# Performance work log

Measured on AMD Instinct MI355X. Metric: run time of the kernel, lower is better.

Reference implementation:

```python
import jax, jax.numpy as jnp
import numpy as np

N_NODES = 50000
N_EDGES = 300000
N_GRAPHS = 256
F_IN = 78
H1 = 10
F_H1 = 78
F_OUT = 128
NEG_SLOPE = 0.2  # PyG GATConv default leaky_relu slope


def gat_conv(x, src, dst, W, a_src, a_dst, bias, heads, out_dim):
    """PyG GATConv (eval mode): linear -> per-edge attention -> segment softmax over
    destination nodes -> scatter-add aggregation -> concat heads + bias.
    src/dst already include self-loops."""
    N = x.shape[0]
    h = (x @ W).reshape(N, heads, out_dim)              # [N,H,F]
    al_s = (h * a_src[None]).sum(-1)                     # [N,H]
    al_d = (h * a_dst[None]).sum(-1)                     # [N,H]
    e = jax.nn.leaky_relu(al_s[src] + al_d[dst], NEG_SLOPE)  # [E,H]
    m = jax.ops.segment_max(e, dst, num_segments=N)      # stable softmax per dst node
    w = jnp.exp(e - m[dst])
    denom = jax.ops.segment_sum(w, dst, num_segments=N)
    alpha = w / denom[dst]                               # [E,H]
    out = jax.ops.segment_sum(h[src] * alpha[:, :, None], dst, num_segments=N)
    return out.reshape(N, heads * out_dim) + bias


def setup_inputs() -> dict:
    key = jax.random.key(0)
    ks = jax.random.split(key, 16)
    x = jax.random.normal(ks[0], (N_NODES, F_IN), dtype=jnp.float32)
    edge_index = jax.random.randint(ks[1], (2, N_EDGES), 0, N_NODES, dtype=jnp.int32)
    batch = jnp.sort(jax.random.randint(ks[2], (N_NODES,), 0, N_GRAPHS, dtype=jnp.int32))
    s = 0.1
    W1 = jax.random.normal(ks[3], (F_IN, H1 * F_H1), dtype=jnp.float32) * s
    a_src1 = jax.random.normal(ks[4], (H1, F_H1), dtype=jnp.float32) * s
    a_dst1 = jax.random.normal(ks[5], (H1, F_H1), dtype=jnp.float32) * s
    b1 = jnp.zeros((H1 * F_H1,), dtype=jnp.float32)
    W2 = jax.random.normal(ks[6], (H1 * F_H1, F_OUT), dtype=jnp.float32) * s
    a_src2 = jax.random.normal(ks[7], (1, F_OUT), dtype=jnp.float32) * s
    a_dst2 = jax.random.normal(ks[8], (1, F_OUT), dtype=jnp.float32) * s
    b2 = jnp.zeros((F_OUT,), dtype=jnp.float32)
    fc_w = jax.random.normal(ks[9], (F_OUT, F_OUT), dtype=jnp.float32) * s
    fc_b = jnp.zeros((F_OUT,), dtype=jnp.float32)
    return dict(x=x, edge_index=edge_index, batch=batch, W1=W1, a_src1=a_src1,
                a_dst1=a_dst1, b1=b1, W2=W2, a_src2=a_src2, a_dst2=a_dst2, b2=b2,
                fc_w=fc_w, fc_b=fc_b)


def reference(x, edge_index, batch, W1, a_src1, a_dst1, b1, W2, a_src2, a_dst2, b2, fc_w, fc_b):
    N = x.shape[0]
    loop = jnp.arange(N, dtype=edge_index.dtype)
    src = jnp.concatenate([edge_index[0], loop])  # add self-loops (PyG default)
    dst = jnp.concatenate([edge_index[1], loop])
    # dropout layers are identity in eval mode
    h = jax.nn.elu(gat_conv(x, src, dst, W1, a_src1, a_dst1, b1, H1, F_H1))
    h = gat_conv(h, src, dst, W2, a_src2, a_dst2, b2, 1, F_OUT)
    h = jax.nn.relu(h)
    g = jax.ops.segment_max(h, batch, num_segments=N_GRAPHS)  # global max pool [B,F]
    out = jax.nn.relu(g @ fc_w + fc_b)
    return out
```

## Files before the change

kernel.cpp:

```cpp
#include <hip/hip_runtime.h>
#include <hip/hip_bf16.h>

#define N_NODES 50000
#define N_EDGES 300000
#define E_TOT   350000
#define N_GRAPHS 256
#define F_IN 78
#define H1 10
#define D1 780
#define F_OUT 128
#define KP 800
#define K1P 96
#define O1P 808
#define NEG_SLOPE 0.2f
#define NB 196

typedef float v4f __attribute__((ext_vector_type(4)));
typedef short v8s __attribute__((ext_vector_type(8)));

__device__ __forceinline__ int src_of(int e, const int* __restrict__ ei) {
  return (e < N_EDGES) ? ei[e] : (e - N_EDGES);
}
__device__ __forceinline__ int dst_of(int e, const int* __restrict__ ei) {
  return (e < N_EDGES) ? ei[N_EDGES + e] : (e - N_EDGES);
}
__device__ __forceinline__ float bf2f(unsigned short u) {
  return __uint_as_float(((unsigned int)u) << 16);
}


__global__ void k_deg(const int* __restrict__ ei, int* __restrict__ deg) {
  int e = blockIdx.x * 256 + threadIdx.x;
  if (e >= E_TOT) return;
  atomicAdd(&deg[dst_of(e, ei)], 1);
}

__global__ void k_scan1(const int* __restrict__ deg, int* __restrict__ part) {
  __shared__ int s[256];
  int t = threadIdx.x;
  int i = blockIdx.x * 256 + t;
  s[t] = (i < N_NODES) ? deg[i] : 0;
  __syncthreads();
  for (int d = 128; d > 0; d >>= 1) {
    if (t < d) s[t] += s[t + d];
    __syncthreads();
  }
  if (t == 0) part[blockIdx.x] = s[0];
}

__global__ void k_scan2(const int* __restrict__ part, int* __restrict__ ppref) {
  if (threadIdx.x == 0) {
    int run = 0;
    for (int i = 0; i < NB; ++i) { ppref[i] = run; run += part[i]; }
  }
}

__global__ void k_scan3(const int* __restrict__ deg, const int* __restrict__ ppref,
                        int* __restrict__ offs, int* __restrict__ cursor) {
  __shared__ int s[256];
  int t = threadIdx.x;
  int i = blockIdx.x * 256 + t;
  int v = (i < N_NODES) ? deg[i] : 0;
  s[t] = v;
  __syncthreads();
  for (int d = 1; d < 256; d <<= 1) {
    int u = (t >= d) ? s[t - d] : 0;
    __syncthreads();
    s[t] += u;
    __syncthreads();
  }
  int excl = s[t] - v;
  if (i < N_NODES) {
    int off = ppref[blockIdx.x] + excl;
    offs[i] = off;
    cursor[i] = off;
  }
}

__global__ void k_scatter(const int* __restrict__ ei, int* __restrict__ cursor,
                          int* __restrict__ src_s, int* __restrict__ dst_s) {
  int e = blockIdx.x * 256 + threadIdx.x;
  if (e >= E_TOT) return;
  int s = src_of(e, ei);
  int d = dst_of(e, ei);
  int pos = atomicAdd(&cursor[d], 1);
  src_s[pos] = s;
  dst_s[pos] = d;
}


__global__ void k_xb(const float* __restrict__ x, __hip_bfloat16* __restrict__ xb) {
  int i = blockIdx.x * 256 + threadIdx.x;
  if (i >= N_NODES * F_IN) return;
  xb[i] = __float2bfloat16(x[i]);
}


__global__ void k_prep(const float* __restrict__ W1, const float* __restrict__ as1,
                       const float* __restrict__ ad1, float* __restrict__ was,
                       float* __restrict__ wad) {
  int i = blockIdx.x * 256 + threadIdx.x;
  if (i >= F_IN * H1) return;
  int k = i / H1, h = i - k * H1;
  const float* wrow = W1 + (size_t)k * D1 + h * 78;
  const float* ar = as1 + h * 78;
  const float* br = ad1 + h * 78;
  float s = 0.f, d = 0.f;
  for (int f = 0; f < 78; ++f) {
    float w = wrow[f];
    s = fmaf(w, ar[f], s);
    d = fmaf(w, br[f], d);
  }
  was[i] = s;
  wad[i] = d;
}


__global__ __launch_bounds__(320) void k_logits1(const float* __restrict__ x,
                                                 const float* __restrict__ was,
                                                 const float* __restrict__ wad,
                                                 float* __restrict__ als,
                                                 float* __restrict__ ald) {
  __shared__ float xs[32][81];
  __shared__ float wl[D1], wl2[D1];
  int tid = threadIdx.x;
  int n0 = blockIdx.x * 32;
  for (int i = tid; i < 32 * F_IN; i += 320) {
    int r = i / F_IN, k = i - r * F_IN;
    int n = n0 + r;
    xs[r][k] = (n < N_NODES) ? x[(size_t)n * F_IN + k] : 0.f;
  }
  for (int i = tid; i < D1; i += 320) { wl[i] = was[i]; wl2[i] = wad[i]; }
  __syncthreads();
  int r = tid / 10, h = tid - r * 10;
  int n = n0 + r;
  float s = 0.f, d = 0.f;
  for (int k = 0; k < F_IN; ++k) {
    float xv = xs[r][k];
    s = fmaf(xv, wl[k * 10 + h], s);
    d = fmaf(xv, wl2[k * 10 + h], d);
  }
  if (n < N_NODES) { als[n * 10 + h] = s; ald[n * 10 + h] = d; }
}


__global__ void k_w1e(const float* __restrict__ als1, const float* __restrict__ ald1,
                      const int* __restrict__ src_s, const int* __restrict__ dst_s,
                      float* __restrict__ w1) {
  int i = blockIdx.x * 256 + threadIdx.x;
  if (i >= E_TOT * H1) return;
  int pos = i / H1, h = i - pos * H1;
  float v = als1[src_s[pos] * H1 + h] + ald1[dst_s[pos] * H1 + h];
  v = (v > 0.f) ? v : NEG_SLOPE * v;
  w1[i] = __expf(v);
}


__global__ void k_w1t(const float* __restrict__ W1, __hip_bfloat16* __restrict__ T) {
  int i = blockIdx.x * 256 + threadIdx.x;
  if (i >= 800 * K1P) return;
  int r = i / K1P, k = i - r * K1P;
  float v = (r < D1 && k < F_IN) ? W1[(size_t)k * D1 + r] : 0.f;
  T[i] = __float2bfloat16(v);
}


__global__ void k_w2t(const float* __restrict__ W2, __hip_bfloat16* __restrict__ Bt) {
  int i = blockIdx.x * 256 + threadIdx.x;
  if (i >= F_OUT * KP) return;
  int c = i / KP, k = i - c * KP;
  float v = (k < D1) ? W2[(size_t)k * F_OUT + c] : 0.f;
  Bt[i] = __float2bfloat16(v);
}


__global__ __launch_bounds__(512, 4) void k_l12(const __hip_bfloat16* __restrict__ xb16,
                                                const float* __restrict__ w1,
                                                const int* __restrict__ src_s,
                                                const int* __restrict__ offs,
                                                const int* __restrict__ deg,
                                                const __hip_bfloat16* __restrict__ W1T,
                                                const float* __restrict__ b1,
                                                const __hip_bfloat16* __restrict__ W2T,
                                                const float* __restrict__ a_src2,
                                                const float* __restrict__ a_dst2,
                                                __hip_bfloat16* __restrict__ h2b,
                                                float* __restrict__ als2,
                                                float* __restrict__ ald2) {
  __shared__ __align__(16) unsigned char lds[34048];
  __hip_bfloat16* xbb = (__hip_bfloat16*)lds;
  __hip_bfloat16* out1t = (__hip_bfloat16*)lds;
  float* h2t = (float*)(lds + 25856);
#define XB(h, g, k) xbb[((h) * 16 + (g)) * 104 + (k)]

  int tid = threadIdx.x, wid = tid >> 6, lane = tid & 63;
  int n0 = blockIdx.x * 16;
  int col16 = lane & 15, kq = (lane >> 4) * 8;

  {
    unsigned int* p = (unsigned int*)lds;
    for (int i = tid; i < H1 * 16 * 52; i += 512) p[i] = 0u;
  }
  __syncthreads();

  #pragma unroll
  for (int rep = 0; rep < 2; ++rep) {
    int g = wid * 2 + rep;
    int n = n0 + g;
    int o = __builtin_amdgcn_readfirstlane(offs[n]);
    int d = __builtin_amdgcn_readfirstlane(deg[n]);
    float acc[H1], acc2[H1];
    #pragma unroll
    for (int h = 0; h < H1; ++h) { acc[h] = 0.f; acc2[h] = 0.f; }

    float onesel = (lane == 14) ? 1.0f : 0.f;
    const unsigned short* xu = (const unsigned short*)xb16;
    int j = 0;
    for (; j + 4 <= d; j += 4) {
      int e0 = o + j;
      int s0 = src_s[e0], s1 = src_s[e0 + 1], s2 = src_s[e0 + 2], s3 = src_s[e0 + 3];
      const unsigned short* x0 = xu + (size_t)s0 * F_IN;
      const unsigned short* x1 = xu + (size_t)s1 * F_IN;
      const unsigned short* x2 = xu + (size_t)s2 * F_IN;
      const unsigned short* x3 = xu + (size_t)s3 * F_IN;
      float xa0 = bf2f(x0[lane]), xa1 = bf2f(x1[lane]);
      float xa2 = bf2f(x2[lane]), xa3 = bf2f(x3[lane]);
      float xb0 = (lane < 14) ? bf2f(x0[64 + lane]) : onesel;
      float xb1 = (lane < 14) ? bf2f(x1[64 + lane]) : onesel;
      float xb2 = (lane < 14) ? bf2f(x2[64 + lane]) : onesel;
      float xb3 = (lane < 14) ? bf2f(x3[64 + lane]) : onesel;
      const float* wp = w1 + (size_t)e0 * H1;
      #pragma unroll
      for (int h = 0; h < H1; ++h) {
        float wa = wp[h], wb = wp[10 + h], wc = wp[20 + h], wd = wp[30 + h];
        acc[h] = fmaf(wa, xa0, acc[h]);
        acc[h] = fmaf(wb, xa1, acc[h]);
        acc[h] = fmaf(wc, xa2, acc[h]);
        acc[h] = fmaf(wd, xa3, acc[h]);
        acc2[h] = fmaf(wa, xb0, acc2[h]);
        acc2[h] = fmaf(wb, xb1, acc2[h]);
        acc2[h] = fmaf(wc, xb2, acc2[h]);
        acc2[h] = fmaf(wd, xb3, acc2[h]);
      }
    }
    for (; j < d; ++j) {
      int e0 = o + j;
      int s0 = src_s[e0];
      const unsigned short* x0 = xu + (size_t)s0 * F_IN;
      float xa0 = bf2f(x0[lane]);
      float xb0 = (lane < 14) ? bf2f(x0[64 + lane]) : onesel;
      const float* wp = w1 + (size_t)e0 * H1;
      #pragma unroll
      for (int h = 0; h < H1; ++h) {
        float wa = wp[h];
        acc[h] = fmaf(wa, xa0, acc[h]);
        acc2[h] = fmaf(wa, xb0, acc2[h]);
      }
    }
    #pragma unroll
    for (int h = 0; h < H1; ++h) {
      float inv = 1.f / __shfl(acc2[h], 14);
      XB(h, g, lane) = __float2bfloat16(acc[h] * inv);
      if (lane < 14) XB(h, g, 64 + lane) = __float2bfloat16(acc2[h] * inv);
    }
  }
  __syncthreads();

  const unsigned short* Bp1 = (const unsigned short*)W1T;
  v4f res[7];
  #pragma unroll
  for (int i = 0; i < 7; ++i) {
    int u = wid + i * 8;
    v4f acc = (v4f){0.f, 0.f, 0.f, 0.f};
    if (u < 50) {
      int h = u / 5, nt = u - (u / 5) * 5;
      #pragma unroll
      for (int kt = 0; kt < 3; ++kt) {
        v8s a = *reinterpret_cast<const v8s*>(&XB(h, col16, kt * 32 + kq));
        v8s b = *reinterpret_cast<const v8s*>(
            &Bp1[(size_t)(h * 78 + nt * 16 + col16) * K1P + kt * 32 + kq]);
        acc = __builtin_amdgcn_mfma_f32_16x16x32_bf16(a, b, acc, 0, 0, 0);
      }
    }
    res[i] = acc;
  }
  __syncthreads();

  if (tid < 224) {
    int node = tid / 14, cc = (tid - node * 14) * 2;
    *(unsigned int*)&out1t[node * O1P + 780 + cc] = 0u;
  }
  #pragma unroll
  for (int i = 0; i < 7; ++i) {
    int u = wid + i * 8;
    if (u < 50) {
      int h = u / 5, nt = u - (u / 5) * 5;
      v4f acc = res[i];
      int cl = nt * 16 + col16;
      if (cl < 78) {
        int c = h * 78 + cl;
        float bv = b1[c];
        #pragma unroll
        for (int r = 0; r < 4; ++r) {
          int node = (lane >> 4) * 4 + r;
          float v = acc[r] + bv;
          v = (v > 0.f) ? v : expm1f(v);
          out1t[node * O1P + c] = __float2bfloat16(v);
        }
      }
    }
  }
  __syncthreads();

  const unsigned short* Bp2 = (const unsigned short*)W2T;
  v4f acc3 = (v4f){0.f, 0.f, 0.f, 0.f};
  #pragma unroll 5
  for (int kt = 0; kt < 25; ++kt) {
    int k = kt * 32 + kq;
    v8s a = *reinterpret_cast<const v8s*>(&out1t[col16 * O1P + k]);
    v8s b = *reinterpret_cast<const v8s*>(&Bp2[(size_t)(wid * 16 + col16) * KP + k]);
    acc3 = __builtin_amdgcn_mfma_f32_16x16x32_bf16(a, b, acc3, 0, 0, 0);
  }
  {
    int col = wid * 16 + col16;
    #pragma unroll
    for (int r = 0; r < 4; ++r) {
      int node = (lane >> 4) * 4 + r;
      h2b[(size_t)(n0 + node) * F_OUT + col] = __float2bfloat16(acc3[r]);
      h2t[node * F_OUT + col] = acc3[r];
    }
  }
  __syncthreads();

  #pragma unroll
  for (int rep = 0; rep < 2; ++rep) {
    int nn = wid * 2 + rep;
    float v0 = h2t[nn * F_OUT + lane], v1 = h2t[nn * F_OUT + 64 + lane];
    float s = v0 * a_src2[lane] + v1 * a_src2[64 + lane];
    float dd = v0 * a_dst2[lane] + v1 * a_dst2[64 + lane];
    #pragma unroll
    for (int off = 32; off > 0; off >>= 1) {
      s += __shfl_down(s, off);
      dd += __shfl_down(dd, off);
    }
    if (lane == 0) { als2[n0 + nn] = s; ald2[n0 + nn] = dd; }
  }
#undef XB
}


__global__ void k_w2e(const float* __restrict__ als2, const float* __restrict__ ald2,
                      const int* __restrict__ src_s, const int* __restrict__ dst_s,
                      float* __restrict__ w2) {
  int pos = blockIdx.x * 256 + threadIdx.x;
  if (pos >= E_TOT) return;
  float v = als2[src_s[pos]] + ald2[dst_s[pos]];
  v = (v > 0.f) ? v : NEG_SLOPE * v;
  w2[pos] = __expf(v);
}


__global__ __launch_bounds__(512) void k_agg2f(const __hip_bfloat16* __restrict__ h2b,
                                               const float* __restrict__ w2,
                                               const int* __restrict__ src_s,
                                               const int* __restrict__ offs,
                                               const int* __restrict__ deg,
                                               const float* __restrict__ b2,
                                               const int* __restrict__ batch,
                                               unsigned int* __restrict__ g) {
  int tid = threadIdx.x;
  int n = blockIdx.x * 4 + (tid >> 7);
  int f = tid & 127;
  int o = __builtin_amdgcn_readfirstlane(offs[n]);
  int d = __builtin_amdgcn_readfirstlane(deg[n]);
  const unsigned short* hu = (const unsigned short*)h2b;
  float acc = 0.f, ssum = 0.f;
  int j = 0;
  for (; j + 4 <= d; j += 4) {
    float wq[4], hq[4];
    #pragma unroll
    for (int q = 0; q < 4; ++q) {
      int e = o + j + q;
      wq[q] = w2[e];
      hq[q] = bf2f(hu[(size_t)src_s[e] * F_OUT + f]);
    }
    #pragma unroll
    for (int q = 0; q < 4; ++q) {
      ssum += wq[q];
      acc = fmaf(wq[q], hq[q], acc);
    }
  }
  for (; j < d; ++j) {
    int e = o + j;
    float w = w2[e];
    ssum += w;
    acc = fmaf(w, bf2f(hu[(size_t)src_s[e] * F_OUT + f]), acc);
  }
  float v = fmaxf(acc / ssum + b2[f], 0.f);
  int gc = __builtin_amdgcn_readfirstlane(batch[n]);
  atomicMax(&g[gc * F_OUT + f], __float_as_uint(v));
}


__global__ __launch_bounds__(128) void k_fc(const float* __restrict__ g,
                                            const float* __restrict__ fc_w,
                                            const float* __restrict__ fc_b,
                                            float* __restrict__ out) {
  int b = blockIdx.x, c = threadIdx.x;
  const float* gr = g + (size_t)b * F_OUT;
  float acc = 0.f;
  for (int k = 0; k < F_OUT; ++k) acc = fmaf(gr[k], fc_w[k * F_OUT + c], acc);
  float v = acc + fc_b[c];
  out[(size_t)b * F_OUT + c] = fmaxf(v, 0.f);
}


extern "C" void kernel_launch(void* const* d_in, const int* in_sizes, int n_in,
                              void* d_out, int out_size, void* d_ws, size_t ws_size,
                              hipStream_t stream) {
  const float* x      = (const float*)d_in[0];
  const int*   ei     = (const int*)  d_in[1];
  const int*   batch  = (const int*)  d_in[2];
  const float* W1     = (const float*)d_in[3];
  const float* a_src1 = (const float*)d_in[4];
  const float* a_dst1 = (const float*)d_in[5];
  const float* b1     = (const float*)d_in[6];
  const float* W2     = (const float*)d_in[7];
  const float* a_src2 = (const float*)d_in[8];
  const float* a_dst2 = (const float*)d_in[9];
  const float* b2     = (const float*)d_in[10];
  const float* fc_w   = (const float*)d_in[11];
  const float* fc_b   = (const float*)d_in[12];
  float* out = (float*)d_out;

  float* ws = (float*)d_ws;
  __hip_bfloat16* h2b = (__hip_bfloat16*)ws;
  float* als1 = ws + 3200000;
  float* ald1 = ws + 3700000;
  float* als2 = ws + 4200000;
  float* ald2 = ws + 4250000;
  float* g    = ws + 4300000;
  float* was  = ws + 4333000;
  float* wad  = ws + 4334000;
  __hip_bfloat16* W2T = (__hip_bfloat16*)(ws + 4335000);
  __hip_bfloat16* W1T = (__hip_bfloat16*)(ws + 4387000);
  __hip_bfloat16* xb16 = (__hip_bfloat16*)(ws + 4426000);
  float* w1   = ws + 6377000;
  float* w2   = ws + 9877000;
  int* ib     = (int*)(ws + 10227000);
  int* deg    = ib;
  int* offs   = ib + 50000;
  int* cursor = ib + 100000;
  int* src_s  = ib + 150000;
  int* dst_s  = ib + 500000;
  int* part   = ib + 850000;
  int* ppref  = ib + 850224;

  hipMemsetAsync(deg, 0, N_NODES * sizeof(int), stream);
  k_deg<<<(E_TOT + 255) / 256, 256, 0, stream>>>(ei, deg);
  k_scan1<<<NB, 256, 0, stream>>>(deg, part);
  k_scan2<<<1, 64, 0, stream>>>(part, ppref);
  k_scan3<<<NB, 256, 0, stream>>>(deg, ppref, offs, cursor);
  k_scatter<<<(E_TOT + 255) / 256, 256, 0, stream>>>(ei, cursor, src_s, dst_s);

  k_prep<<<4, 256, 0, stream>>>(W1, a_src1, a_dst1, was, wad);
  k_w1t<<<(800 * K1P + 255) / 256, 256, 0, stream>>>(W1, W1T);
  k_w2t<<<(F_OUT * KP + 255) / 256, 256, 0, stream>>>(W2, W2T);
  k_xb<<<(N_NODES * F_IN + 255) / 256, 256, 0, stream>>>(x, xb16);
  hipMemsetAsync(g, 0, N_GRAPHS * F_OUT * sizeof(float), stream);

  k_logits1<<<(N_NODES + 31) / 32, 320, 0, stream>>>(x, was, wad, als1, ald1);
  k_w1e<<<(E_TOT * H1 + 255) / 256, 256, 0, stream>>>(als1, ald1, src_s, dst_s, w1);

  k_l12<<<N_NODES / 16, 512, 0, stream>>>(xb16, w1, src_s, offs, deg, W1T, b1,
                                          W2T, a_src2, a_dst2, h2b, als2, ald2);

  k_w2e<<<(E_TOT + 255) / 256, 256, 0, stream>>>(als2, ald2, src_s, dst_s, w2);
  k_agg2f<<<(N_NODES + 3) / 4, 512, 0, stream>>>(h2b, w2, src_s, offs, deg, b2, batch, (unsigned int*)g);

  k_fc<<<N_GRAPHS, F_OUT, 0, stream>>>(g, fc_w, fc_b, out);
}
```

Before: 311.6 us.

## Fuse layer-2 edge weights into aggregation and pack bf16 neighbor feature loads

Removes the separate k_w2e kernel and its w2 buffer. k_agg2f now computes the leaky-relu and exp edge weight inline from als2 of the source and ald2 of the destination, saving a launch and a per-edge global write and read. In the layer-1 gather, each lane loads one 32-bit word holding two bf16 features instead of two 16-bit loads. A constant 1.0 in lane 39 produces the softmax denominator, and results go to LDS as packed pairs. The h2t LDS tile is padded to a 132-float stride to reduce bank conflicts. The cost is that exp is now recomputed per feature thread in the aggregation, which is redundant across the 128 threads of a node.

```diff
diff --git a/kernel.cpp b/kernel.cpp
--- a/kernel.cpp
+++ b/kernel.cpp
@@ -12,6 +12,8 @@
 #define KP 800
 #define K1P 96
 #define O1P 808
+#define H2P 132
+#define XROW 39
 #define NEG_SLOPE 0.2f
 #define NB 196
 
@@ -26,6 +28,10 @@
 }
 __device__ __forceinline__ float bf2f(unsigned short u) {
   return __uint_as_float(((unsigned int)u) << 16);
+}
+__device__ __forceinline__ unsigned short f2bf(float f) {
+  __hip_bfloat16 b = __float2bfloat16(f);
+  return *reinterpret_cast<unsigned short*>(&b);
 }
 
 
@@ -187,7 +193,7 @@
                                                 __hip_bfloat16* __restrict__ h2b,
                                                 float* __restrict__ als2,
                                                 float* __restrict__ ald2) {
-  __shared__ __align__(16) unsigned char lds[34048];
+  __shared__ __align__(16) unsigned char lds[34304];
   __hip_bfloat16* xbb = (__hip_bfloat16*)lds;
   __hip_bfloat16* out1t = (__hip_bfloat16*)lds;
   float* h2t = (float*)(lds + 25856);
@@ -203,65 +209,67 @@
   }
   __syncthreads();
 
+  const unsigned int* xu = (const unsigned int*)xb16;
+  bool ldl = lane < XROW;
+  const unsigned int onesu = 0x00003F80u;
   #pragma unroll
   for (int rep = 0; rep < 2; ++rep) {
     int g = wid * 2 + rep;
     int n = n0 + g;
     int o = __builtin_amdgcn_readfirstlane(offs[n]);
     int d = __builtin_amdgcn_readfirstlane(deg[n]);
-    float acc[H1], acc2[H1];
-    #pragma unroll
-    for (int h = 0; h < H1; ++h) { acc[h] = 0.f; acc2[h] = 0.f; }
-
-    float onesel = (lane == 14) ? 1.0f : 0.f;
-    const unsigned short* xu = (const unsigned short*)xb16;
+    float accLo[H1], accHi[H1];
+    #pragma unroll
+    for (int h = 0; h < H1; ++h) { accLo[h] = 0.f; accHi[h] = 0.f; }
+
     int j = 0;
     for (; j + 4 <= d; j += 4) {
       int e0 = o + j;
       int s0 = src_s[e0], s1 = src_s[e0 + 1], s2 = src_s[e0 + 2], s3 = src_s[e0 + 3];
-      const unsigned short* x0 = xu + (size_t)s0 * F_IN;
-      const unsigned short* x1 = xu + (size_t)s1 * F_IN;
-      const unsigned short* x2 = xu + (size_t)s2 * F_IN;
-      const unsigned short* x3 = xu + (size_t)s3 * F_IN;
-      float xa0 = bf2f(x0[lane]), xa1 = bf2f(x1[lane]);
-      float xa2 = bf2f(x2[lane]), xa3 = bf2f(x3[lane]);
-      float xb0 = (lane < 14) ? bf2f(x0[64 + lane]) : onesel;
-      float xb1 = (lane < 14) ? bf2f(x1[64 + lane]) : onesel;
-      float xb2 = (lane < 14) ? bf2f(x2[64 + lane]) : onesel;
-      float xb3 = (lane < 14) ? bf2f(x3[64 + lane]) : onesel;
+      unsigned int u0 = ldl ? xu[(size_t)s0 * XROW + lane] : onesu;
+      unsigned int u1 = ldl ? xu[(size_t)s1 * XROW + lane] : onesu;
+      unsigned int u2 = ldl ? xu[(size_t)s2 * XROW + lane] : onesu;
+      unsigned int u3 = ldl ? xu[(size_t)s3 * XROW + lane] : onesu;
+      float lo0 = __uint_as_float(u0 << 16), hi0 = __uint_as_float(u0 & 0xFFFF0000u);
+      float lo1 = __uint_as_float(u1 << 16), hi1 = __uint_as_float(u1 & 0xFFFF0000u);
+      float lo2 = __uint_as_float(u2 << 16), hi2 = __uint_as_float(u2 & 0xFFFF0000u);
+      float lo3 = __uint_as_float(u3 << 16), hi3 = __uint_as_float(u3 & 0xFFFF0000u);
       const float* wp = w1 + (size_t)e0 * H1;
       #pragma unroll
       for (int h = 0; h < H1; ++h) {
         float wa = wp[h], wb = wp[10 + h], wc = wp[20 + h], wd = wp[30 + h];
-        acc[h] = fmaf(wa, xa0, acc[h]);
-        acc[h] = fmaf(wb, xa1, acc[h]);
-        acc[h] = fmaf(wc, xa2, acc[h]);
-        acc[h] = fmaf(wd, xa3, acc[h]);
-        acc2[h] = fmaf(wa, xb0, acc2[h]);
-        acc2[h] = fmaf(wb, xb1, acc2[h]);
-        acc2[h] = fmaf(wc, xb2, acc2[h]);
-        acc2[h] = fmaf(wd, xb3, acc2[h]);
+        accLo[h] = fmaf(wa, lo0, accLo[h]);
+        accLo[h] = fmaf(wb, lo1, accLo[h]);
+        accLo[h] = fmaf(wc, lo2, accLo[h]);
+        accLo[h] = fmaf(wd, lo3, accLo[h]);
+        accHi[h] = fmaf(wa, hi0, accHi[h]);
+        accHi[h] = fmaf(wb, hi1, accHi[h]);
+        accHi[h] = fmaf(wc, hi2, accHi[h]);
+        accHi[h] = fmaf(wd, hi3, accHi[h]);
       }
     }
     for (; j < d; ++j) {
       int e0 = o + j;
       int s0 = src_s[e0];
-      const unsigned short* x0 = xu + (size_t)s0 * F_IN;
-      float xa0 = bf2f(x0[lane]);
-      float xb0 = (lane < 14) ? bf2f(x0[64 + lane]) : onesel;
+      unsigned int u0 = ldl ? xu[(size_t)s0 * XROW + lane] : onesu;
+      float lo0 = __uint_as_float(u0 << 16), hi0 = __uint_as_float(u0 & 0xFFFF0000u);
       const float* wp = w1 + (size_t)e0 * H1;
       #pragma unroll
       for (int h = 0; h < H1; ++h) {
         float wa = wp[h];
-        acc[h] = fmaf(wa, xa0, acc[h]);
-        acc2[h] = fmaf(wa, xb0, acc2[h]);
+        accLo[h] = fmaf(wa, lo0, accLo[h]);
+        accHi[h] = fmaf(wa, hi0, accHi[h]);
       }
     }
     #pragma unroll
     for (int h = 0; h < H1; ++h) {
-      float inv = 1.f / __shfl(acc2[h], 14);
-      XB(h, g, lane) = __float2bfloat16(acc[h] * inv);
-      if (lane < 14) XB(h, g, 64 + lane) = __float2bfloat16(acc2[h] * inv);
+      float inv = 1.f / __shfl(accLo[h], XROW);
+      if (ldl) {
+        unsigned int pk = (unsigned int)f2bf(accLo[h] * inv)
+                        | ((unsigned int)f2bf(accHi[h] * inv) << 16);
+        *reinterpret_cast<unsigned int*>(
+            reinterpret_cast<unsigned char*>(&XB(h, g, 0)) + 4 * lane) = pk;
+      }
     }
   }
   __syncthreads();
@@ -327,7 +335,7 @@
     for (int r = 0; r < 4; ++r) {
       int node = (lane >> 4) * 4 + r;
       h2b[(size_t)(n0 + node) * F_OUT + col] = __float2bfloat16(acc3[r]);
-      h2t[node * F_OUT + col] = acc3[r];
+      h2t[node * H2P + col] = acc3[r];
     }
   }
   __syncthreads();
@@ -335,7 +343,7 @@
   #pragma unroll
   for (int rep = 0; rep < 2; ++rep) {
     int nn = wid * 2 + rep;
-    float v0 = h2t[nn * F_OUT + lane], v1 = h2t[nn * F_OUT + 64 + lane];
+    float v0 = h2t[nn * H2P + lane], v1 = h2t[nn * H2P + 64 + lane];
     float s = v0 * a_src2[lane] + v1 * a_src2[64 + lane];
     float dd = v0 * a_dst2[lane] + v1 * a_dst2[64 + lane];
     #pragma unroll
@@ -349,19 +357,9 @@
 }
 
 
-__global__ void k_w2e(const float* __restrict__ als2, const float* __restrict__ ald2,
-                      const int* __restrict__ src_s, const int* __restrict__ dst_s,
-                      float* __restrict__ w2) {
-  int pos = blockIdx.x * 256 + threadIdx.x;
-  if (pos >= E_TOT) return;
-  float v = als2[src_s[pos]] + ald2[dst_s[pos]];
-  v = (v > 0.f) ? v : NEG_SLOPE * v;
-  w2[pos] = __expf(v);
-}
-
-
 __global__ __launch_bounds__(512) void k_agg2f(const __hip_bfloat16* __restrict__ h2b,
-                                               const float* __restrict__ w2,
+                                               const float* __restrict__ als2,
+                                               const float* __restrict__ ald2,
                                                const int* __restrict__ src_s,
                                                const int* __restrict__ offs,
                                                const int* __restrict__ deg,
@@ -373,6 +371,7 @@
   int f = tid & 127;
   int o = __builtin_amdgcn_readfirstlane(offs[n]);
   int d = __builtin_amdgcn_readfirstlane(deg[n]);
+  float aldn = ald2[n];
   const unsigned short* hu = (const unsigned short*)h2b;
   float acc = 0.f, ssum = 0.f;
   int j = 0;
@@ -381,8 +380,11 @@
     #pragma unroll
     for (int q = 0; q < 4; ++q) {
       int e = o + j + q;
-      wq[q] = w2[e];
-      hq[q] = bf2f(hu[(size_t)src_s[e] * F_OUT + f]);
+      int sb = src_s[e];
+      float v = als2[sb] + aldn;
+      v = (v > 0.f) ? v : NEG_SLOPE * v;
+      wq[q] = __expf(v);
+      hq[q] = bf2f(hu[(size_t)sb * F_OUT + f]);
     }
     #pragma unroll
     for (int q = 0; q < 4; ++q) {
@@ -392,9 +394,12 @@
   }
   for (; j < d; ++j) {
     int e = o + j;
-    float w = w2[e];
+    int sb = src_s[e];
+    float v = als2[sb] + aldn;
+    v = (v > 0.f) ? v : NEG_SLOPE * v;
+    float w = __expf(v);
     ssum += w;
-    acc = fmaf(w, bf2f(hu[(size_t)src_s[e] * F_OUT + f]), acc);
+    acc = fmaf(w, bf2f(hu[(size_t)sb * F_OUT + f]), acc);
   }
   float v = fmaxf(acc / ssum + b2[f], 0.f);
   int gc = __builtin_amdgcn_readfirstlane(batch[n]);
@@ -446,8 +451,7 @@
   __hip_bfloat16* W1T = (__hip_bfloat16*)(ws + 4387000);
   __hip_bfloat16* xb16 = (__hip_bfloat16*)(ws + 4426000);
   float* w1   = ws + 6377000;
-  float* w2   = ws + 9877000;
-  int* ib     = (int*)(ws + 10227000);
+  int* ib     = (int*)(ws + 9877000);
   int* deg    = ib;
   int* offs   = ib + 50000;
   int* cursor = ib + 100000;
@@ -475,8 +479,8 @@
   k_l12<<<N_NODES / 16, 512, 0, stream>>>(xb16, w1, src_s, offs, deg, W1T, b1,
                                           W2T, a_src2, a_dst2, h2b, als2, ald2);
 
-  k_w2e<<<(E_TOT + 255) / 256, 256, 0, stream>>>(als2, ald2, src_s, dst_s, w2);
-  k_agg2f<<<(N_NODES + 3) / 4, 512, 0, stream>>>(h2b, w2, src_s, offs, deg, b2, batch, (unsigned int*)g);
+  k_agg2f<<<(N_NODES + 3) / 4, 512, 0, stream>>>(h2b, als2, ald2, src_s, offs, deg,
+                                                 b2, batch, (unsigned int*)g);
 
   k_fc<<<N_GRAPHS, F_OUT, 0, stream>>>(g, fc_w, fc_b, out);
 }
```

New measurement: 295.3 us. 1.05x faster.
